# Performance work log

Hardware: AMD Instinct MI355X
Metric: run time of the kernel (lower is better)

Reference implementation:

```python
import jax, jax.numpy as jnp
import numpy as np

B, S = 32, 4096
Q_DIM, KV_DIM, A_DIM = 512, 512, 128


def setup_inputs() -> dict:
    key = jax.random.key(0)
    k1, k2, k3, k4, k5, k6 = jax.random.split(key, 6)
    query = jax.random.normal(k1, (B, Q_DIM), dtype=jnp.float32)
    kv = jax.random.normal(k2, (B, S, KV_DIM), dtype=jnp.float32)
    mask = jax.random.randint(k3, (B, S), 0, 2).astype(bool)
    # learned params (torch Linear(in, out, bias=False) stores W as [out, in]; we apply x @ W.T)
    Wq = jax.random.normal(k4, (A_DIM, Q_DIM), dtype=jnp.float32) / np.sqrt(Q_DIM)
    Wk = jax.random.normal(k5, (A_DIM, KV_DIM), dtype=jnp.float32) / np.sqrt(KV_DIM)
    Ws = jax.random.normal(k6, (1, A_DIM), dtype=jnp.float32) / np.sqrt(A_DIM)
    return {"query": query, "kv": kv, "mask": mask, "Wq": Wq, "Wk": Wk, "Ws": Ws}


def reference(query, kv, mask, Wq, Wk, Ws):
    # q: [B, 1, A], k: [B, S, A]
    q = jnp.einsum('bq,aq->ba', query, Wq)[:, None, :]
    k = jnp.einsum('bsk,ak->bsa', kv, Wk)
    # additive (Bahdanau) scores: [B, S]
    scores = jnp.einsum('bsa,a->bs', jnp.tanh(q + k), Ws[0])
    scores = jnp.where(mask, scores, -jnp.inf)
    weights = jax.nn.softmax(scores, axis=-1)
    context = jnp.einsum('bs,bsk->bk', weights, kv)
    return context, weights
```

## Files before the change

### kernel.cpp

```cpp
#include <hip/hip_runtime.h>


typedef __attribute__((ext_vector_type(8))) short short8;
typedef __attribute__((ext_vector_type(4))) float f32x4;

#define S_LEN 4096
#define BATCH 32
#define KVD 512
#define AD 128
#define SCHN 32
#define CHUNKS_PER_B (S_LEN / SCHN)
#define NCHUNK (BATCH * CHUNKS_PER_B)

#define FLAG_OFF   0
#define Q_OFF      1024
#define WK_OFF     17408
#define SCORES_OFF 148480
#define MD_OFF     672768
#define CTXP_OFF   705536
#define SCL_OFF    9094144
#define MD2_OFF    9110528

__device__ __forceinline__ unsigned short f2bf_rne(float f) {
  unsigned int u = __float_as_uint(f);
  u = (u + 0x7FFFu + ((u >> 16) & 1u)) >> 16;
  return (unsigned short)u;
}
__device__ __forceinline__ unsigned int packbf(float a, float b) {
  unsigned int lo = __float_as_uint(a) + 0x8000u;
  unsigned int hi = __float_as_uint(b) + 0x8000u;
  return (lo >> 16) | (hi & 0xFFFF0000u);
}
__device__ __forceinline__ float tanh_fast(float x) {
  return 1.0f - 2.0f / (1.0f + __expf(2.0f * x));
}

__global__ __launch_bounds__(256) void prep_kernel(
    const float* __restrict__ query, const float* __restrict__ Wq,
    const float* __restrict__ Wk, const void* __restrict__ maskp,
    float* __restrict__ qws, unsigned short* __restrict__ wkb,
    int* __restrict__ flagp) {
  int blk = blockIdx.x, t = threadIdx.x;
  if (blk < 32) {
    __shared__ float qrow[KVD];
    qrow[t] = query[blk * KVD + t];
    qrow[t + 256] = query[blk * KVD + t + 256];
    __syncthreads();
    int a = t >> 1, half = t & 1;
    const float4* wq4 = (const float4*)(Wq + (size_t)a * KVD + half * 256);
    const float4* qr4 = (const float4*)(qrow + half * 256);
    float s = 0.f;
#pragma unroll 8
    for (int i = 0; i < 64; ++i) {
      float4 wv = wq4[i], qv = qr4[i];
      s += wv.x * qv.x + wv.y * qv.y + wv.z * qv.z + wv.w * qv.w;
    }
    s += __shfl_xor(s, 1);
    if (half == 0) qws[blk * AD + a] = s;
  } else if (blk < 40) {
    int j = blk - 32;
    const float4* src = (const float4*)Wk;
#pragma unroll 4
    for (int i = 0; i < 8; ++i) {
      int idx4 = j * 2048 + i * 256 + t;
      float4 v = src[idx4];
      ushort4 o;
      o.x = f2bf_rne(v.x); o.y = f2bf_rne(v.y);
      o.z = f2bf_rne(v.z); o.w = f2bf_rne(v.w);
      ((ushort4*)wkb)[idx4] = o;
    }
  } else {
    __shared__ int okv;
    if (t == 0) okv = 1;
    __syncthreads();
    if (t < 128) {
      int wv = ((const int*)maskp)[t];
      if (!(wv == 0 || wv == 1)) okv = 0;
    }
    __syncthreads();
    if (t == 0) flagp[0] = okv;
  }
}

__global__ __launch_bounds__(64) void main_kernel(
    const float* __restrict__ kv, const void* __restrict__ maskp,
    const float* __restrict__ Ws, const float* __restrict__ qws,
    const unsigned short* __restrict__ wkb, const int* __restrict__ flagp,
    float* __restrict__ scores, float* __restrict__ md,
    float* __restrict__ ctxp) {
  int lane = threadIdx.x;
  int g = blockIdx.x;
  int b = g >> 7, chunk = g & (CHUNKS_PER_B - 1);
  int s0 = chunk * SCHN;
  int lr = lane & 15, lg = lane >> 4;

  __shared__ char tileb[SCHN * 1024];
  __shared__ float escf[SCHN];

  int flag = flagp[0];
  int mload = 0;
  if (lane < SCHN) {
    int gs = b * S_LEN + s0 + lane;
    mload = flag ? ((const int*)maskp)[gs]
                 : (int)((const unsigned char*)maskp)[gs];
  }
  float qv[8], wv[8];
#pragma unroll
  for (int n = 0; n < 8; ++n) {
    qv[n] = qws[b * AD + n * 16 + lr];
    wv[n] = Ws[n * 16 + lr];
  }

  const float* src = kv + ((size_t)b * S_LEN + s0) * KVD;
#pragma unroll 8
  for (int r = 0; r < SCHN; ++r) {
    float4 v0 = *(const float4*)(src + (size_t)r * KVD + lane * 4);
    float4 v1 = *(const float4*)(src + (size_t)r * KVD + 256 + lane * 4);
    uint2 w0, w1;
    w0.x = packbf(v0.x, v0.y); w0.y = packbf(v0.z, v0.w);
    w1.x = packbf(v1.x, v1.y); w1.y = packbf(v1.z, v1.w);
    int xr = (r & 7) << 4;
    *(uint2*)(tileb + ((r * 1024 + lane * 8) ^ xr)) = w0;
    *(uint2*)(tileb + ((r * 1024 + 512 + lane * 8) ^ xr)) = w1;
  }
  __syncthreads();

  f32x4 acc[2][8];
#pragma unroll
  for (int mi = 0; mi < 2; ++mi)
#pragma unroll
    for (int n = 0; n < 8; ++n) acc[mi][n] = (f32x4)0.f;

  const unsigned short* brow = wkb + (size_t)lr * KVD + lg * 8;
  const char* ta0 = tileb + lr * 1024;
  const char* ta1 = tileb + (16 + lr) * 1024;
  int axor = (lr & 7) << 4;

  for (int kk = 0; kk < KVD / 32; ++kk) {
    int ko = (kk * 64 + lg * 16) ^ axor;
    short8 af0 = *(const short8*)(ta0 + ko);
    short8 af1 = *(const short8*)(ta1 + ko);
#pragma unroll
    for (int n = 0; n < 8; ++n) {
      short8 bf = *(const short8*)(brow + (size_t)n * 16 * KVD + kk * 32);
      acc[0][n] = __builtin_amdgcn_mfma_f32_16x16x32_bf16(af0, bf, acc[0][n], 0, 0, 0);
      acc[1][n] = __builtin_amdgcn_mfma_f32_16x16x32_bf16(af1, bf, acc[1][n], 0, 0, 0);
    }
  }

  float sc[2][4];
#pragma unroll
  for (int mi = 0; mi < 2; ++mi) {
#pragma unroll
    for (int reg = 0; reg < 4; ++reg) {
      float v = 0.f;
#pragma unroll
      for (int n = 0; n < 8; ++n)
        v += tanh_fast(qv[n] + acc[mi][n][reg]) * wv[n];
      v += __shfl_xor(v, 1);
      v += __shfl_xor(v, 2);
      v += __shfl_xor(v, 4);
      v += __shfl_xor(v, 8);
      int row = 16 * mi + 4 * lg + reg;
      int mk = __shfl(mload, row);
      sc[mi][reg] = mk ? v : -INFINITY;
    }
  }

  float m = -INFINITY;
#pragma unroll
  for (int mi = 0; mi < 2; ++mi)
#pragma unroll
    for (int reg = 0; reg < 4; ++reg) m = fmaxf(m, sc[mi][reg]);
  m = fmaxf(m, __shfl_xor(m, 16));
  m = fmaxf(m, __shfl_xor(m, 32));
  float e[2][4];
  float d = 0.f;
#pragma unroll
  for (int mi = 0; mi < 2; ++mi)
#pragma unroll
    for (int reg = 0; reg < 4; ++reg) {
      e[mi][reg] = (sc[mi][reg] == -INFINITY) ? 0.f : __expf(sc[mi][reg] - m);
      d += e[mi][reg];
    }
  d += __shfl_xor(d, 16);
  d += __shfl_xor(d, 32);

  if (lr == 0) {
#pragma unroll
    for (int mi = 0; mi < 2; ++mi)
#pragma unroll
      for (int reg = 0; reg < 4; ++reg) {
        int row = 16 * mi + 4 * lg + reg;
        escf[row] = e[mi][reg];
        scores[b * S_LEN + s0 + row] = sc[mi][reg];
      }
  }
  if (lane == 0) { md[g * 2] = m; md[g * 2 + 1] = d; }
  __syncthreads();

  float4 c0 = make_float4(0.f, 0.f, 0.f, 0.f);
  float4 c1 = make_float4(0.f, 0.f, 0.f, 0.f);
#pragma unroll 4
  for (int s = 0; s < SCHN; ++s) {
    float ev = escf[s];
    uint4 u = *(const uint4*)(tileb + ((s * 1024 + lane * 16) ^ ((s & 7) << 4)));
    c0.x += ev * __uint_as_float(u.x << 16);
    c0.y += ev * __uint_as_float(u.x & 0xFFFF0000u);
    c0.z += ev * __uint_as_float(u.y << 16);
    c0.w += ev * __uint_as_float(u.y & 0xFFFF0000u);
    c1.x += ev * __uint_as_float(u.z << 16);
    c1.y += ev * __uint_as_float(u.z & 0xFFFF0000u);
    c1.z += ev * __uint_as_float(u.w << 16);
    c1.w += ev * __uint_as_float(u.w & 0xFFFF0000u);
  }
  float* cp = ctxp + (size_t)g * KVD + lane * 8;
  *(float4*)cp = c0;
  *(float4*)(cp + 4) = c1;
}

__global__ __launch_bounds__(128) void combineA_kernel(
    const float* __restrict__ md, float* __restrict__ scl,
    float* __restrict__ md2) {
  int b = blockIdx.x, t = threadIdx.x;
  float mv = md[(b * CHUNKS_PER_B + t) * 2];
  float dv = md[(b * CHUNKS_PER_B + t) * 2 + 1];
  __shared__ float rmax[2], rsum[2];
  float m = mv;
  m = fmaxf(m, __shfl_xor(m, 1));
  m = fmaxf(m, __shfl_xor(m, 2));
  m = fmaxf(m, __shfl_xor(m, 4));
  m = fmaxf(m, __shfl_xor(m, 8));
  m = fmaxf(m, __shfl_xor(m, 16));
  m = fmaxf(m, __shfl_xor(m, 32));
  if ((t & 63) == 0) rmax[t >> 6] = m;
  __syncthreads();
  float M = fmaxf(rmax[0], rmax[1]);
  float e = (dv > 0.f) ? __expf(mv - M) : 0.f;
  float pd = e * dv;
  pd += __shfl_xor(pd, 1);
  pd += __shfl_xor(pd, 2);
  pd += __shfl_xor(pd, 4);
  pd += __shfl_xor(pd, 8);
  pd += __shfl_xor(pd, 16);
  pd += __shfl_xor(pd, 32);
  if ((t & 63) == 0) rsum[t >> 6] = pd;
  __syncthreads();
  float D = rsum[0] + rsum[1];
  float invD = 1.f / D;
  scl[b * CHUNKS_PER_B + t] = e * invD;
  if (t == 0) { md2[b * 2] = M; md2[b * 2 + 1] = invD; }
}

__global__ __launch_bounds__(256) void combineB_kernel(
    const float* __restrict__ scl, const float* __restrict__ md2,
    const float* __restrict__ ctxp, const float* __restrict__ scores,
    float* __restrict__ out) {
  int strip = blockIdx.x, b = blockIdx.y, t = threadIdx.x;
  if (strip < 8) {
    __shared__ float part[4][64];
    int c = strip * 64 + (t & 63);
    int jg = t >> 6;
    float sum = 0.f;
    for (int j = jg; j < CHUNKS_PER_B; j += 4)
      sum += scl[b * CHUNKS_PER_B + j] *
             ctxp[(size_t)(b * CHUNKS_PER_B + j) * KVD + c];
    part[jg][t & 63] = sum;
    __syncthreads();
    if (t < 64)
      out[b * KVD + c] = part[0][t] + part[1][t] + part[2][t] + part[3][t];
  } else {
    float M = md2[b * 2], invD = md2[b * 2 + 1];
    int sbase = (strip - 8) * 1024;
#pragma unroll
    for (int i = 0; i < 4; ++i) {
      int s = sbase + i * 256 + t;
      float scv = scores[b * S_LEN + s];
      out[BATCH * KVD + b * S_LEN + s] = __expf(scv - M) * invD;
    }
  }
}

extern "C" void kernel_launch(void* const* d_in, const int* in_sizes, int n_in,
                              void* d_out, int out_size, void* d_ws, size_t ws_size,
                              hipStream_t stream) {
  const float* query = (const float*)d_in[0];
  const float* kv    = (const float*)d_in[1];
  const void*  maskp = d_in[2];
  const float* Wq    = (const float*)d_in[3];
  const float* Wk    = (const float*)d_in[4];
  const float* Ws    = (const float*)d_in[5];
  float* out = (float*)d_out;
  char* w = (char*)d_ws;
  int* flagp = (int*)(w + FLAG_OFF);
  float* qws = (float*)(w + Q_OFF);
  unsigned short* wkb = (unsigned short*)(w + WK_OFF);
  float* scores = (float*)(w + SCORES_OFF);
  float* md = (float*)(w + MD_OFF);
  float* ctxp = (float*)(w + CTXP_OFF);
  float* scl = (float*)(w + SCL_OFF);
  float* md2 = (float*)(w + MD2_OFF);

  prep_kernel<<<41, 256, 0, stream>>>(query, Wq, Wk, maskp, qws, wkb, flagp);
  main_kernel<<<NCHUNK, 64, 0, stream>>>(kv, maskp, Ws, qws, wkb, flagp,
                                         scores, md, ctxp);
  combineA_kernel<<<BATCH, 128, 0, stream>>>(md, scl, md2);
  combineB_kernel<<<dim3(12, BATCH), 256, 0, stream>>>(scl, md2, ctxp, scores, out);
}
```

Baseline: 134.9 us.

## Load kv fragments directly from global and split chunk across two waves

Removes the 32KB LDS staging tile. Each of two waves in a 128-thread block now handles 16 rows, loading MFMA A-fragments straight from global fp32 kv and converting them to bf16 in registers. The weighted context sum re-reads kv from global in fp32, relying on cache hits, instead of the bf16 LDS copy. The two waves merge their softmax partials and context sums through shared memory before writing one partial per block. This lowers LDS use and raises occupancy, at the cost of a second global read pass over kv and strided, less coalesced fragment loads.

```diff
diff --git a/kernel.cpp b/kernel.cpp
--- a/kernel.cpp
+++ b/kernel.cpp
@@ -8,9 +8,8 @@
 #define BATCH 32
 #define KVD 512
 #define AD 128
-#define SCHN 32
-#define CHUNKS_PER_B (S_LEN / SCHN)
-#define NCHUNK (BATCH * CHUNKS_PER_B)
+#define CHUNKS_PER_B 128
+#define NPAIR (BATCH * CHUNKS_PER_B)
 
 #define FLAG_OFF   0
 #define Q_OFF      1024
@@ -82,24 +81,26 @@
   }
 }
 
-__global__ __launch_bounds__(64) void main_kernel(
+__global__ __launch_bounds__(128) void main_kernel(
     const float* __restrict__ kv, const void* __restrict__ maskp,
     const float* __restrict__ Ws, const float* __restrict__ qws,
     const unsigned short* __restrict__ wkb, const int* __restrict__ flagp,
     float* __restrict__ scores, float* __restrict__ md,
     float* __restrict__ ctxp) {
-  int lane = threadIdx.x;
-  int g = blockIdx.x;
-  int b = g >> 7, chunk = g & (CHUNKS_PER_B - 1);
-  int s0 = chunk * SCHN;
+  int t = threadIdx.x;
+  int lane = t & 63, wave = t >> 6;
+  int g2 = blockIdx.x;
+  int b = g2 >> 7, pr = g2 & (CHUNKS_PER_B - 1);
+  int s0 = pr * 32 + wave * 16;
   int lr = lane & 15, lg = lane >> 4;
 
-  __shared__ char tileb[SCHN * 1024];
-  __shared__ float escf[SCHN];
+  __shared__ float mrg[KVD];
+  __shared__ float mdsh[2][2];
+  __shared__ float escf[2][16];
 
   int flag = flagp[0];
   int mload = 0;
-  if (lane < SCHN) {
+  if (lane < 16) {
     int gs = b * S_LEN + s0 + lane;
     mload = flag ? ((const int*)maskp)[gs]
                  : (int)((const unsigned char*)maskp)[gs];
@@ -111,112 +112,107 @@
     wv[n] = Ws[n * 16 + lr];
   }
 
-  const float* src = kv + ((size_t)b * S_LEN + s0) * KVD;
-#pragma unroll 8
-  for (int r = 0; r < SCHN; ++r) {
-    float4 v0 = *(const float4*)(src + (size_t)r * KVD + lane * 4);
-    float4 v1 = *(const float4*)(src + (size_t)r * KVD + 256 + lane * 4);
-    uint2 w0, w1;
-    w0.x = packbf(v0.x, v0.y); w0.y = packbf(v0.z, v0.w);
-    w1.x = packbf(v1.x, v1.y); w1.y = packbf(v1.z, v1.w);
-    int xr = (r & 7) << 4;
-    *(uint2*)(tileb + ((r * 1024 + lane * 8) ^ xr)) = w0;
-    *(uint2*)(tileb + ((r * 1024 + 512 + lane * 8) ^ xr)) = w1;
-  }
-  __syncthreads();
-
-  f32x4 acc[2][8];
-#pragma unroll
-  for (int mi = 0; mi < 2; ++mi)
-#pragma unroll
-    for (int n = 0; n < 8; ++n) acc[mi][n] = (f32x4)0.f;
-
+  f32x4 acc[8];
+#pragma unroll
+  for (int n = 0; n < 8; ++n) acc[n] = (f32x4)0.f;
+
+  const float* arow = kv + ((size_t)b * S_LEN + s0 + lr) * KVD + lg * 8;
   const unsigned short* brow = wkb + (size_t)lr * KVD + lg * 8;
-  const char* ta0 = tileb + lr * 1024;
-  const char* ta1 = tileb + (16 + lr) * 1024;
-  int axor = (lr & 7) << 4;
-
+
+#pragma unroll 2
   for (int kk = 0; kk < KVD / 32; ++kk) {
-    int ko = (kk * 64 + lg * 16) ^ axor;
-    short8 af0 = *(const short8*)(ta0 + ko);
-    short8 af1 = *(const short8*)(ta1 + ko);
+    float4 alo = *(const float4*)(arow + kk * 32);
+    float4 ahi = *(const float4*)(arow + kk * 32 + 4);
+    short8 af;
+    ((unsigned int*)&af)[0] = packbf(alo.x, alo.y);
+    ((unsigned int*)&af)[1] = packbf(alo.z, alo.w);
+    ((unsigned int*)&af)[2] = packbf(ahi.x, ahi.y);
+    ((unsigned int*)&af)[3] = packbf(ahi.z, ahi.w);
 #pragma unroll
     for (int n = 0; n < 8; ++n) {
       short8 bf = *(const short8*)(brow + (size_t)n * 16 * KVD + kk * 32);
-      acc[0][n] = __builtin_amdgcn_mfma_f32_16x16x32_bf16(af0, bf, acc[0][n], 0, 0, 0);
-      acc[1][n] = __builtin_amdgcn_mfma_f32_16x16x32_bf16(af1, bf, acc[1][n], 0, 0, 0);
-    }
-  }
-
-  float sc[2][4];
-#pragma unroll
-  for (int mi = 0; mi < 2; ++mi) {
-#pragma unroll
-    for (int reg = 0; reg < 4; ++reg) {
-      float v = 0.f;
-#pragma unroll
-      for (int n = 0; n < 8; ++n)
-        v += tanh_fast(qv[n] + acc[mi][n][reg]) * wv[n];
-      v += __shfl_xor(v, 1);
-      v += __shfl_xor(v, 2);
-      v += __shfl_xor(v, 4);
-      v += __shfl_xor(v, 8);
-      int row = 16 * mi + 4 * lg + reg;
-      int mk = __shfl(mload, row);
-      sc[mi][reg] = mk ? v : -INFINITY;
-    }
-  }
-
-  float m = -INFINITY;
-#pragma unroll
-  for (int mi = 0; mi < 2; ++mi)
-#pragma unroll
-    for (int reg = 0; reg < 4; ++reg) m = fmaxf(m, sc[mi][reg]);
+      acc[n] = __builtin_amdgcn_mfma_f32_16x16x32_bf16(af, bf, acc[n], 0, 0, 0);
+    }
+  }
+
+  float sc[4];
+#pragma unroll
+  for (int reg = 0; reg < 4; ++reg) {
+    float v = 0.f;
+#pragma unroll
+    for (int n = 0; n < 8; ++n)
+      v += tanh_fast(qv[n] + acc[n][reg]) * wv[n];
+    v += __shfl_xor(v, 1);
+    v += __shfl_xor(v, 2);
+    v += __shfl_xor(v, 4);
+    v += __shfl_xor(v, 8);
+    int row = 4 * lg + reg;
+    int mk = __shfl(mload, row);
+    sc[reg] = mk ? v : -INFINITY;
+  }
+
+  float m = fmaxf(fmaxf(sc[0], sc[1]), fmaxf(sc[2], sc[3]));
   m = fmaxf(m, __shfl_xor(m, 16));
   m = fmaxf(m, __shfl_xor(m, 32));
-  float e[2][4];
-  float d = 0.f;
-#pragma unroll
-  for (int mi = 0; mi < 2; ++mi)
-#pragma unroll
-    for (int reg = 0; reg < 4; ++reg) {
-      e[mi][reg] = (sc[mi][reg] == -INFINITY) ? 0.f : __expf(sc[mi][reg] - m);
-      d += e[mi][reg];
-    }
+  float e[4], d = 0.f;
+#pragma unroll
+  for (int reg = 0; reg < 4; ++reg) {
+    e[reg] = (sc[reg] == -INFINITY) ? 0.f : __expf(sc[reg] - m);
+    d += e[reg];
+  }
   d += __shfl_xor(d, 16);
   d += __shfl_xor(d, 32);
 
   if (lr == 0) {
 #pragma unroll
-    for (int mi = 0; mi < 2; ++mi)
-#pragma unroll
-      for (int reg = 0; reg < 4; ++reg) {
-        int row = 16 * mi + 4 * lg + reg;
-        escf[row] = e[mi][reg];
-        scores[b * S_LEN + s0 + row] = sc[mi][reg];
-      }
-  }
-  if (lane == 0) { md[g * 2] = m; md[g * 2 + 1] = d; }
-  __syncthreads();
+    for (int reg = 0; reg < 4; ++reg) {
+      escf[wave][4 * lg + reg] = e[reg];
+      scores[b * S_LEN + s0 + 4 * lg + reg] = sc[reg];
+    }
+  }
+  if (lane == 0) { mdsh[wave][0] = m; mdsh[wave][1] = d; }
 
   float4 c0 = make_float4(0.f, 0.f, 0.f, 0.f);
   float4 c1 = make_float4(0.f, 0.f, 0.f, 0.f);
+  const float* kvc = kv + ((size_t)b * S_LEN + s0) * KVD + lane * 8;
 #pragma unroll 4
-  for (int s = 0; s < SCHN; ++s) {
-    float ev = escf[s];
-    uint4 u = *(const uint4*)(tileb + ((s * 1024 + lane * 16) ^ ((s & 7) << 4)));
-    c0.x += ev * __uint_as_float(u.x << 16);
-    c0.y += ev * __uint_as_float(u.x & 0xFFFF0000u);
-    c0.z += ev * __uint_as_float(u.y << 16);
-    c0.w += ev * __uint_as_float(u.y & 0xFFFF0000u);
-    c1.x += ev * __uint_as_float(u.z << 16);
-    c1.y += ev * __uint_as_float(u.z & 0xFFFF0000u);
-    c1.z += ev * __uint_as_float(u.w << 16);
-    c1.w += ev * __uint_as_float(u.w & 0xFFFF0000u);
-  }
-  float* cp = ctxp + (size_t)g * KVD + lane * 8;
-  *(float4*)cp = c0;
-  *(float4*)(cp + 4) = c1;
+  for (int s = 0; s < 16; ++s) {
+    float ev = escf[wave][s];
+    float4 v0 = *(const float4*)(kvc + (size_t)s * KVD);
+    float4 v1 = *(const float4*)(kvc + (size_t)s * KVD + 4);
+    c0.x += ev * v0.x; c0.y += ev * v0.y; c0.z += ev * v0.z; c0.w += ev * v0.w;
+    c1.x += ev * v1.x; c1.y += ev * v1.y; c1.z += ev * v1.z; c1.w += ev * v1.w;
+  }
+
+  __syncthreads();
+  float m0 = mdsh[0][0], d0 = mdsh[0][1];
+  float m1 = mdsh[1][0], d1 = mdsh[1][1];
+  float M = fmaxf(m0, m1);
+  float scl0 = (d0 > 0.f) ? __expf(m0 - M) : 0.f;
+  float scl1 = (d1 > 0.f) ? __expf(m1 - M) : 0.f;
+  float D = scl0 * d0 + scl1 * d1;
+
+  if (wave == 0) {
+    float4 w0, w1;
+    w0.x = scl0 * c0.x; w0.y = scl0 * c0.y; w0.z = scl0 * c0.z; w0.w = scl0 * c0.w;
+    w1.x = scl0 * c1.x; w1.y = scl0 * c1.y; w1.z = scl0 * c1.z; w1.w = scl0 * c1.w;
+    *(float4*)&mrg[lane * 8] = w0;
+    *(float4*)&mrg[lane * 8 + 4] = w1;
+  }
+  __syncthreads();
+  if (wave == 1) {
+    float4 r0 = *(const float4*)&mrg[lane * 8];
+    float4 r1 = *(const float4*)&mrg[lane * 8 + 4];
+    r0.x += scl1 * c0.x; r0.y += scl1 * c0.y; r0.z += scl1 * c0.z; r0.w += scl1 * c0.w;
+    r1.x += scl1 * c1.x; r1.y += scl1 * c1.y; r1.z += scl1 * c1.z; r1.w += scl1 * c1.w;
+    float* cp = ctxp + (size_t)g2 * KVD + lane * 8;
+    *(float4*)cp = r0;
+    *(float4*)(cp + 4) = r1;
+    if (lane == 0) {
+      md[g2 * 2] = (D > 0.f) ? M : -INFINITY;
+      md[g2 * 2 + 1] = D;
+    }
+  }
 }
 
 __global__ __launch_bounds__(128) void combineA_kernel(
@@ -302,7 +298,7 @@
   float* md2 = (float*)(w + MD2_OFF);
 
   prep_kernel<<<41, 256, 0, stream>>>(query, Wq, Wk, maskp, qws, wkb, flagp);
-  main_kernel<<<NCHUNK, 64, 0, stream>>>(kv, maskp, Ws, qws, wkb, flagp,
+  main_kernel<<<NPAIR, 128, 0, stream>>>(kv, maskp, Ws, qws, wkb, flagp,
                                          scores, md, ctxp);
   combineA_kernel<<<BATCH, 128, 0, stream>>>(md, scl, md2);
   combineB_kernel<<<dim3(12, BATCH), 256, 0, stream>>>(scl, md2, ctxp, scores, out);
```

Result: slower. 223.6 us (+65.8%).
